# Performance work log

Hardware: AMD Instinct MI355X
Metric: run time of the kernel (lower is better)

## Reference

```python
import jax, jax.numpy as jnp
import numpy as np

NODELEN = 394
N_NODES = 50000
N_EDGES = 200000
IN_DIM = 2 * NODELEN  # 788
H2 = 192
EMB = 128


def setup_inputs() -> dict:
    key = jax.random.key(0)
    ks = jax.random.split(key, 12)
    inp = {
        'features': jax.random.normal(ks[0], (N_NODES, NODELEN), dtype=jnp.float32),
        'src': jax.random.randint(ks[1], (N_EDGES,), 0, N_NODES),
        'dst': jax.random.randint(ks[2], (N_EDGES,), 0, N_NODES),
        # AutoEncoder params (Linear weights stored as [in, out])
        'W_enc1': jax.random.normal(ks[3], (IN_DIM, H2), dtype=jnp.float32) / np.sqrt(IN_DIM),
        'b_enc1': jnp.zeros((H2,), dtype=jnp.float32),
        'W_enc3': jax.random.normal(ks[4], (H2, EMB), dtype=jnp.float32) / np.sqrt(H2),
        'b_enc3': jnp.zeros((EMB,), dtype=jnp.float32),
        'W_dec1': jax.random.normal(ks[5], (EMB, H2), dtype=jnp.float32) / np.sqrt(EMB),
        'b_dec1': jnp.zeros((H2,), dtype=jnp.float32),
        'W_dec3': jax.random.normal(ks[6], (H2, IN_DIM), dtype=jnp.float32) / np.sqrt(H2),
        'b_dec3': jnp.zeros((IN_DIM,), dtype=jnp.float32),
    }
    return inp


def _segment_mean(msgs, dst, inv_deg, n):
    # msgs: [E, F] gathered neighbor features; mean over incoming edges per node
    return jax.ops.segment_sum(msgs, dst, num_segments=n) * inv_deg


def reference(features, src, dst, W_enc1, b_enc1, W_enc3, b_enc3,
              W_dec1, b_dec1, W_dec3, b_dec3):
    n = features.shape[0]
    ones = jnp.ones(src.shape[0], dtype=features.dtype)
    deg = jax.ops.segment_sum(ones, dst, num_segments=n)
    # nodes with no neighbors fall back to the zero dummy vector (as in source)
    inv_deg = (1.0 / jnp.maximum(deg, 1.0))[:, None]

    # depth-1 aggregation: mean of raw neighbor features, then feat[0] := 0
    h1 = _segment_mean(features[src], dst, inv_deg, n)
    h1 = h1.at[:, 0].set(0.0)
    # depth-2 aggregation: mean of depth-1 aggregates of neighbors, feat[0] := 0
    h2 = _segment_mean(h1[src], dst, inv_deg, n)
    h2 = h2.at[:, 0].set(0.0)

    # concatenated embedding with positions 0 and NODELEN zeroed
    emb = jnp.concatenate([features, h2], axis=1)  # [N, 788]
    emb = emb.at[:, 0].set(0.0).at[:, NODELEN].set(0.0)

    # AutoEncoder forward (dropout is identity at inference)
    x = jax.nn.relu(emb @ W_enc1 + b_enc1)
    encoded = x @ W_enc3 + b_enc3
    y = jax.nn.relu(encoded @ W_dec1 + b_dec1)
    decoded = y @ W_dec3 + b_dec3
    return encoded, decoded, emb
```

## Files before the change

kernel.cpp:

```cpp
#include <hip/hip_runtime.h>
#include <hip/hip_bf16.h>

#define NODELEN 394
#define IN_DIM 788
#define H2DIM 192
#define EMBDIM 128
#define NCHUNK 197

typedef __attribute__((ext_vector_type(4))) float f32x4;
typedef __attribute__((ext_vector_type(8))) short bfrag;

#define LBAR() do { asm volatile("s_waitcnt lgkmcnt(0)" ::: "memory"); \
                    __builtin_amdgcn_s_barrier(); } while (0)

static __device__ __forceinline__ unsigned short f2bf(float f) {
    union { float f; unsigned u; } v; v.f = f;
    unsigned r = v.u + 0x7FFFu + ((v.u >> 16) & 1u);
    return (unsigned short)(r >> 16);
}
static __device__ __forceinline__ float bf2f(unsigned short h) {
    union { unsigned u; float f; } v; v.u = ((unsigned)h) << 16;
    return v.f;
}
static __device__ __forceinline__ unsigned short f2bf_fast(float f) {
    __hip_bfloat16 h = __float2bfloat16(f);
    union { __hip_bfloat16 h; unsigned short u; } c; c.h = h; return c.u;
}


__global__ void count_deg(const int* __restrict__ dst, int* __restrict__ deg, int e) {
    int i = blockIdx.x * blockDim.x + threadIdx.x;
    if (i < e) atomicAdd(&deg[dst[i]], 1);
}

__global__ void block_sum(const int* __restrict__ deg, int* __restrict__ bsum, int n) {
    __shared__ int s[256];
    int t = threadIdx.x;
    int i = blockIdx.x * 256 + t;
    s[t] = (i < n) ? deg[i] : 0;
    __syncthreads();
    for (int d = 128; d > 0; d >>= 1) {
        if (t < d) s[t] += s[t + d];
        __syncthreads();
    }
    if (t == 0) bsum[blockIdx.x] = s[0];
}

__global__ void scan_bsums(int* bsum, int nb) {
    __shared__ int s[256];
    int t = threadIdx.x;
    int x0 = (t < nb) ? bsum[t] : 0;
    s[t] = x0;
    __syncthreads();
    for (int d = 1; d < 256; d <<= 1) {
        int u = (t >= d) ? s[t - d] : 0;
        __syncthreads();
        s[t] += u;
        __syncthreads();
    }
    if (t < nb) bsum[t] = s[t] - x0;
}

__global__ void block_scan(const int* __restrict__ deg, const int* __restrict__ boff,
                           int* __restrict__ rowstart, int* __restrict__ cursor,
                           float* __restrict__ inv, int n) {
    __shared__ int s[256];
    int t = threadIdx.x;
    int i = blockIdx.x * 256 + t;
    int x0 = (i < n) ? deg[i] : 0;
    s[t] = x0;
    __syncthreads();
    for (int d = 1; d < 256; d <<= 1) {
        int u = (t >= d) ? s[t - d] : 0;
        __syncthreads();
        s[t] += u;
        __syncthreads();
    }
    if (i < n) {
        int r = boff[blockIdx.x] + s[t] - x0;
        rowstart[i] = r;
        cursor[i] = r;
        inv[i] = 1.0f / fmaxf((float)x0, 1.0f);
    }
}

__global__ void fill_edges(const int* __restrict__ src, const int* __restrict__ dst,
                           int* __restrict__ cursor, int* __restrict__ elist, int e) {
    int i = blockIdx.x * blockDim.x + threadIdx.x;
    if (i < e) {
        int p = atomicAdd(&cursor[dst[i]], 1);
        elist[p] = src[i];
    }
}


__global__ __launch_bounds__(256) void gather1(
        const float* __restrict__ feat, const int* __restrict__ rowstart,
        const int* __restrict__ deg, const float* __restrict__ inv,
        const int* __restrict__ elist, unsigned short* __restrict__ h1) {
    const int node = blockIdx.x;
    const int c = threadIdx.x;
    if (c >= NCHUNK) return;
    const int beg = rowstart[node];
    const int dc = deg[node];
    const float s = inv[node];
    const size_t off = (size_t)c * 2;

    float ax = 0.f, ay = 0.f, bx = 0.f, by = 0.f;
    float cx = 0.f, cy = 0.f, dx = 0.f, dy = 0.f;
    int j = 0;
    for (; j + 3 < dc; j += 4) {
        int n0 = elist[beg + j], n1 = elist[beg + j + 1];
        int n2 = elist[beg + j + 2], n3 = elist[beg + j + 3];
        float2 v0 = *(const float2*)(feat + (size_t)n0 * NODELEN + off);
        float2 v1 = *(const float2*)(feat + (size_t)n1 * NODELEN + off);
        float2 v2 = *(const float2*)(feat + (size_t)n2 * NODELEN + off);
        float2 v3 = *(const float2*)(feat + (size_t)n3 * NODELEN + off);
        ax += v0.x; ay += v0.y; bx += v1.x; by += v1.y;
        cx += v2.x; cy += v2.y; dx += v3.x; dy += v3.y;
    }
    for (; j < dc; ++j) {
        int n0 = elist[beg + j];
        float2 v0 = *(const float2*)(feat + (size_t)n0 * NODELEN + off);
        ax += v0.x; ay += v0.y;
    }
    float fx = (ax + bx + cx + dx) * s;
    float fy = (ay + by + cy + dy) * s;
    if (c == 0) fx = 0.f;
    unsigned out = ((unsigned)f2bf(fy) << 16) | (unsigned)f2bf(fx);
    *(unsigned*)(h1 + (size_t)node * NODELEN + off) = out;
}

__global__ __launch_bounds__(256) void gather2_emb(
        const float* __restrict__ feat, const unsigned* __restrict__ h1,
        const int* __restrict__ rowstart, const int* __restrict__ deg,
        const float* __restrict__ inv, const int* __restrict__ elist,
        float* __restrict__ emb, unsigned* __restrict__ emb16u) {
    const int node = blockIdx.x;
    const int c = threadIdx.x;
    if (c >= NCHUNK) return;
    const int beg = rowstart[node];
    const int dc = deg[node];
    const float s = inv[node];

    float ax = 0.f, ay = 0.f, bx = 0.f, by = 0.f;
    float cx = 0.f, cy = 0.f, dx = 0.f, dy = 0.f;
    int j = 0;
    for (; j + 3 < dc; j += 4) {
        int n0 = elist[beg + j], n1 = elist[beg + j + 1];
        int n2 = elist[beg + j + 2], n3 = elist[beg + j + 3];
        unsigned u0 = h1[(size_t)n0 * NCHUNK + c];
        unsigned u1 = h1[(size_t)n1 * NCHUNK + c];
        unsigned u2 = h1[(size_t)n2 * NCHUNK + c];
        unsigned u3 = h1[(size_t)n3 * NCHUNK + c];
        ax += bf2f((unsigned short)u0); ay += bf2f((unsigned short)(u0 >> 16));
        bx += bf2f((unsigned short)u1); by += bf2f((unsigned short)(u1 >> 16));
        cx += bf2f((unsigned short)u2); cy += bf2f((unsigned short)(u2 >> 16));
        dx += bf2f((unsigned short)u3); dy += bf2f((unsigned short)(u3 >> 16));
    }
    for (; j < dc; ++j) {
        int n0 = elist[beg + j];
        unsigned u0 = h1[(size_t)n0 * NCHUNK + c];
        ax += bf2f((unsigned short)u0); ay += bf2f((unsigned short)(u0 >> 16));
    }
    float hx = (ax + bx + cx + dx) * s;
    float hy = (ay + by + cy + dy) * s;

    const float* fr = feat + (size_t)node * NODELEN;
    float* er = emb + (size_t)node * IN_DIM;
    float2 fv = *(const float2*)(fr + c * 2);
    if (c == 0) { fv.x = 0.f; hx = 0.f; }
    *(float2*)(er + c * 2) = fv;
    float2 hv; hv.x = hx; hv.y = hy;
    *(float2*)(er + NODELEN + c * 2) = hv;

    if (emb16u) {
        unsigned* e16 = emb16u + (size_t)node * 400;
        e16[c]          = ((unsigned)f2bf(fv.y) << 16) | (unsigned)f2bf(fv.x);
        e16[NCHUNK + c] = ((unsigned)f2bf(hy)  << 16) | (unsigned)f2bf(hx);
        if (c < 6) e16[394 + c] = 0u;
    }
}

__device__ __forceinline__ void tr_one(const float* W, unsigned short* Wt,
                                       int K, int N, int Kp, int idx) {
    int nrow = idx / Kp, k = idx - nrow * Kp;
    Wt[idx] = (k < K) ? f2bf(W[(size_t)k * N + nrow]) : (unsigned short)0;
}

#define T1E (192 * 800)
#define T2E (128 * 192)
#define T3E (192 * 128)
#define T4E (788 * 192)

__global__ void transpose_all(const float* __restrict__ W1, unsigned short* __restrict__ Wt1,
                              const float* __restrict__ W2, unsigned short* __restrict__ Wt2,
                              const float* __restrict__ W3, unsigned short* __restrict__ Wt3,
                              const float* __restrict__ W4, unsigned short* __restrict__ Wt4) {
    int idx = blockIdx.x * 256 + threadIdx.x;
    if (idx < T1E) { tr_one(W1, Wt1, IN_DIM, H2DIM, 800, idx); return; }
    idx -= T1E;
    if (idx < T2E) { tr_one(W2, Wt2, H2DIM, EMBDIM, 192, idx); return; }
    idx -= T2E;
    if (idx < T3E) { tr_one(W3, Wt3, EMBDIM, H2DIM, 128, idx); return; }
    idx -= T3E;
    if (idx < T4E) { tr_one(W4, Wt4, H2DIM, IN_DIM, 192, idx); return; }
}

static __device__ __forceinline__ int bs_addr(int r, int s) {
    return r * 32 + ((s ^ ((r >> 1) & 3)) << 3);
}
static __device__ __forceinline__ int xy_base(int r, int s) {
    int ph = (s & 24) | ((s ^ r) & 7);
    return r * 192 + (ph << 3);
}
static __device__ __forceinline__ int xy_addr_s(int r, int col) { return xy_base(r, col >> 3) + (col & 7); }

static __device__ __forceinline__ bfrag load_af_bf(const unsigned short* A800, int gm, int M, int col) {
    const bfrag zf = {0, 0, 0, 0, 0, 0, 0, 0};
    return (gm < M) ? *(const bfrag*)(A800 + (size_t)gm * 800 + col) : zf;
}
static __device__ __forceinline__ bfrag load_af_f32(const float* A, int gm, int M, int col) {
    float t[8];
    #pragma unroll
    for (int q = 0; q < 8; ++q) t[q] = 0.f;
    if (gm < M) {
        const float* rp = A + (size_t)gm * IN_DIM;
        if (col + 8 <= IN_DIM) {
            float4 v0 = *(const float4*)(rp + col), v1 = *(const float4*)(rp + col + 4);
            t[0] = v0.x; t[1] = v0.y; t[2] = v0.z; t[3] = v0.w;
            t[4] = v1.x; t[5] = v1.y; t[6] = v1.z; t[7] = v1.w;
        } else {
            #pragma unroll
            for (int q = 0; q < 8; ++q) if (col + q < IN_DIM) t[q] = rp[col + q];
        }
    }
    union { unsigned short u[8]; bfrag v; } pk;
    #pragma unroll
    for (int q = 0; q < 8; ++q) pk.u[q] = f2bf_fast(t[q]);
    return pk.v;
}

template <int ABF>
__global__ __launch_bounds__(256, 2) void mlp12(
    const void* __restrict__ Aemb,
    const unsigned short* __restrict__ Wt1,
    const unsigned short* __restrict__ Wt2,
    const float* __restrict__ b1, const float* __restrict__ b2,
    float* __restrict__ encoded, unsigned short* __restrict__ enc16, int M)
{
    __shared__ unsigned short XY[128 * 192];
    __shared__ unsigned short Bs[2][192 * 32];

    const int tid = threadIdx.x;
    const int wid = tid >> 6, l = tid & 63;
    const int wm = wid >> 1, wn = wid & 1;
    const int lr = l & 15, lk = l >> 4;
    const int m0 = blockIdx.x * 128;

    const int r0 = tid >> 2, s0 = tid & 3;
    const int r1 = r0 + 64, r2 = r0 + 128;
    const int bw0 = bs_addr(r0, s0);
    const int bw1 = bs_addr(r1, s0);
    const int bw2 = bs_addr(r2, s0);
    int brd6[6], brd4[4];
    #pragma unroll
    for (int j = 0; j < 6; ++j) brd6[j] = bs_addr(wn * 96 + j * 16 + lr, lk);
    #pragma unroll
    for (int j = 0; j < 4; ++j) brd4[j] = bs_addr(wn * 64 + j * 16 + lr, lk);

    int gmA[4];
    #pragma unroll
    for (int i = 0; i < 4; ++i) gmA[i] = m0 + wm * 64 + i * 16 + lr;

    {
        f32x4 acc[4][6];
        #pragma unroll
        for (int i = 0; i < 4; ++i)
            #pragma unroll
            for (int j = 0; j < 6; ++j) acc[i][j] = (f32x4){0.f, 0.f, 0.f, 0.f};

        bfrag afC[4], afN[4], bN[3];
        #pragma unroll
        for (int i = 0; i < 4; ++i)
            afC[i] = ABF ? load_af_bf((const unsigned short*)Aemb, gmA[i], M, lk * 8)
                         : load_af_f32((const float*)Aemb, gmA[i], M, lk * 8);
        *(bfrag*)&Bs[0][bw0] = *(const bfrag*)(Wt1 + (size_t)r0 * 800 + s0 * 8);
        *(bfrag*)&Bs[0][bw1] = *(const bfrag*)(Wt1 + (size_t)r1 * 800 + s0 * 8);
        *(bfrag*)&Bs[0][bw2] = *(const bfrag*)(Wt1 + (size_t)r2 * 800 + s0 * 8);
        LBAR();

        #pragma unroll 5
        for (int kt = 0; kt < 25; ++kt) {
            if (kt < 24) {
                int k0 = (kt + 1) * 32;
                #pragma unroll
                for (int i = 0; i < 4; ++i)
                    afN[i] = ABF ? load_af_bf((const unsigned short*)Aemb, gmA[i], M, k0 + lk * 8)
                                 : load_af_f32((const float*)Aemb, gmA[i], M, k0 + lk * 8);
                bN[0] = *(const bfrag*)(Wt1 + (size_t)r0 * 800 + k0 + s0 * 8);
                bN[1] = *(const bfrag*)(Wt1 + (size_t)r1 * 800 + k0 + s0 * 8);
                bN[2] = *(const bfrag*)(Wt1 + (size_t)r2 * 800 + k0 + s0 * 8);
            }
            const unsigned short* B = Bs[kt & 1];
            bfrag bf[6];
            #pragma unroll
            for (int j = 0; j < 6; ++j) bf[j] = *(const bfrag*)&B[brd6[j]];
            #pragma unroll
            for (int i = 0; i < 4; ++i)
                #pragma unroll
                for (int j = 0; j < 6; ++j)
                    acc[i][j] = __builtin_amdgcn_mfma_f32_16x16x32_bf16(afC[i], bf[j], acc[i][j], 0, 0, 0);
            if (kt < 24) {
                unsigned short* Bn = Bs[(kt + 1) & 1];
                *(bfrag*)&Bn[bw0] = bN[0];
                *(bfrag*)&Bn[bw1] = bN[1];
                *(bfrag*)&Bn[bw2] = bN[2];
                LBAR();
                #pragma unroll
                for (int i = 0; i < 4; ++i) afC[i] = afN[i];
            }
        }
        float bv[6];
        #pragma unroll
        for (int j = 0; j < 6; ++j) bv[j] = b1[wn * 96 + j * 16 + lr];
        #pragma unroll
        for (int i = 0; i < 4; ++i)
            #pragma unroll
            for (int j = 0; j < 6; ++j)
                #pragma unroll
                for (int r = 0; r < 4; ++r) {
                    int m = wm * 64 + i * 16 + lk * 4 + r;
                    int n1 = wn * 96 + j * 16 + lr;
                    XY[xy_addr_s(m, n1)] = f2bf_fast(fmaxf(acc[i][j][r] + bv[j], 0.f));
                }
    }
    __syncthreads();

    {
        f32x4 acc[4][4];
        #pragma unroll
        for (int i = 0; i < 4; ++i)
            #pragma unroll
            for (int j = 0; j < 4; ++j) acc[i][j] = (f32x4){0.f, 0.f, 0.f, 0.f};

        bfrag bN[2];
        *(bfrag*)&Bs[0][bw0] = *(const bfrag*)(Wt2 + (size_t)r0 * 192 + s0 * 8);
        *(bfrag*)&Bs[0][bw1] = *(const bfrag*)(Wt2 + (size_t)r1 * 192 + s0 * 8);
        LBAR();

        #pragma unroll
        for (int kt = 0; kt < 6; ++kt) {
            if (kt < 5) {
                int k0 = (kt + 1) * 32;
                bN[0] = *(const bfrag*)(Wt2 + (size_t)r0 * 192 + k0 + s0 * 8);
                bN[1] = *(const bfrag*)(Wt2 + (size_t)r1 * 192 + k0 + s0 * 8);
            }
            const unsigned short* B = Bs[kt & 1];
            bfrag af[4], bf[4];
            #pragma unroll
            for (int i = 0; i < 4; ++i)
                af[i] = *(const bfrag*)&XY[xy_base(wm * 64 + i * 16 + lr, kt * 4 + lk)];
            #pragma unroll
            for (int j = 0; j < 4; ++j) bf[j] = *(const bfrag*)&B[brd4[j]];
            #pragma unroll
            for (int i = 0; i < 4; ++i)
                #pragma unroll
                for (int j = 0; j < 4; ++j)
                    acc[i][j] = __builtin_amdgcn_mfma_f32_16x16x32_bf16(af[i], bf[j], acc[i][j], 0, 0, 0);
            if (kt < 5) {
                unsigned short* Bn = Bs[(kt + 1) & 1];
                *(bfrag*)&Bn[bw0] = bN[0];
                *(bfrag*)&Bn[bw1] = bN[1];
                LBAR();
            }
        }

        float bv[4];
        #pragma unroll
        for (int j = 0; j < 4; ++j) bv[j] = b2[wn * 64 + j * 16 + lr];
        #pragma unroll
        for (int i = 0; i < 4; ++i)
            #pragma unroll
            for (int j = 0; j < 4; ++j)
                #pragma unroll
                for (int r = 0; r < 4; ++r) {
                    int m = wm * 64 + i * 16 + lk * 4 + r;
                    int nn = wn * 64 + j * 16 + lr;
                    float v = acc[i][j][r] + bv[j];
                    int gm = m0 + m;
                    if (gm < M) {
                        encoded[(size_t)gm * EMBDIM + nn] = v;
                        enc16[(size_t)gm * EMBDIM + nn] = f2bf_fast(v);
                    }
                }
    }
}

__global__ __launch_bounds__(256, 2) void mlp34(
    const unsigned short* __restrict__ enc16,
    const unsigned short* __restrict__ Wt3,
    const unsigned short* __restrict__ Wt4,
    const float* __restrict__ b3, const float* __restrict__ b4,
    float* __restrict__ decoded, int M)
{
    __shared__ unsigned short XY[128 * 192];
    __shared__ unsigned short Bs[2][192 * 32];

    const int tid = threadIdx.x;
    const int wid = tid >> 6, l = tid & 63;
    const int wm = wid >> 1, wn = wid & 1;
    const int lr = l & 15, lk = l >> 4;
    const int m0 = blockIdx.x * 128;
    const bfrag zf = {0, 0, 0, 0, 0, 0, 0, 0};

    const int r0 = tid >> 2, s0 = tid & 3;
    const int r1 = r0 + 64, r2 = r0 + 128;
    const int bw0 = bs_addr(r0, s0);
    const int bw1 = bs_addr(r1, s0);
    const int bw2 = bs_addr(r2, s0);
    int brd6[6], brd4[4];
    #pragma unroll
    for (int j = 0; j < 6; ++j) brd6[j] = bs_addr(wn * 96 + j * 16 + lr, lk);
    #pragma unroll
    for (int j = 0; j < 4; ++j) brd4[j] = bs_addr(wn * 64 + j * 16 + lr, lk);

    int gmA[4];
    #pragma unroll
    for (int i = 0; i < 4; ++i) gmA[i] = m0 + wm * 64 + i * 16 + lr;

    {
        f32x4 acc[4][6];
        #pragma unroll
        for (int i = 0; i < 4; ++i)
            #pragma unroll
            for (int j = 0; j < 6; ++j) acc[i][j] = (f32x4){0.f, 0.f, 0.f, 0.f};

        bfrag afC[4], afN[4], bN[3];
        #pragma unroll
        for (int i = 0; i < 4; ++i)
            afC[i] = (gmA[i] < M) ? *(const bfrag*)(enc16 + (size_t)gmA[i] * EMBDIM + lk * 8) : zf;
        *(bfrag*)&Bs[0][bw0] = *(const bfrag*)(Wt3 + (size_t)r0 * 128 + s0 * 8);
        *(bfrag*)&Bs[0][bw1] = *(const bfrag*)(Wt3 + (size_t)r1 * 128 + s0 * 8);
        *(bfrag*)&Bs[0][bw2] = *(const bfrag*)(Wt3 + (size_t)r2 * 128 + s0 * 8);
        LBAR();

        #pragma unroll
        for (int kt = 0; kt < 4; ++kt) {
            if (kt < 3) {
                int k0 = (kt + 1) * 32;
                #pragma unroll
                for (int i = 0; i < 4; ++i)
                    afN[i] = (gmA[i] < M)
                        ? *(const bfrag*)(enc16 + (size_t)gmA[i] * EMBDIM + k0 + lk * 8) : zf;
                bN[0] = *(const bfrag*)(Wt3 + (size_t)r0 * 128 + k0 + s0 * 8);
                bN[1] = *(const bfrag*)(Wt3 + (size_t)r1 * 128 + k0 + s0 * 8);
                bN[2] = *(const bfrag*)(Wt3 + (size_t)r2 * 128 + k0 + s0 * 8);
            }
            const unsigned short* B = Bs[kt & 1];
            bfrag bf[6];
            #pragma unroll
            for (int j = 0; j < 6; ++j) bf[j] = *(const bfrag*)&B[brd6[j]];
            #pragma unroll
            for (int i = 0; i < 4; ++i)
                #pragma unroll
                for (int j = 0; j < 6; ++j)
                    acc[i][j] = __builtin_amdgcn_mfma_f32_16x16x32_bf16(afC[i], bf[j], acc[i][j], 0, 0, 0);
            if (kt < 3) {
                unsigned short* Bn = Bs[(kt + 1) & 1];
                *(bfrag*)&Bn[bw0] = bN[0];
                *(bfrag*)&Bn[bw1] = bN[1];
                *(bfrag*)&Bn[bw2] = bN[2];
                LBAR();
                #pragma unroll
                for (int i = 0; i < 4; ++i) afC[i] = afN[i];
            }
        }

        float bv[6];
        #pragma unroll
        for (int j = 0; j < 6; ++j) bv[j] = b3[wn * 96 + j * 16 + lr];
        #pragma unroll
        for (int i = 0; i < 4; ++i)
            #pragma unroll
            for (int j = 0; j < 6; ++j)
                #pragma unroll
                for (int r = 0; r < 4; ++r) {
                    int m = wm * 64 + i * 16 + lk * 4 + r;
                    int nc = wn * 96 + j * 16 + lr;
                    XY[xy_addr_s(m, nc)] = f2bf_fast(fmaxf(acc[i][j][r] + bv[j], 0.f));
                }
    }
    __syncthreads();

    {
        bfrag af4[6][4];
        #pragma unroll
        for (int q = 0; q < 6; ++q)
            #pragma unroll
            for (int i = 0; i < 4; ++i)
                af4[q][i] = *(const bfrag*)&XY[xy_base(wm * 64 + i * 16 + lr, q * 4 + lk)];

        bfrag bN[2];
        *(bfrag*)&Bs[0][bw0] = *(const bfrag*)(Wt4 + (size_t)r0 * 192 + s0 * 8);
        *(bfrag*)&Bs[0][bw1] = *(const bfrag*)(Wt4 + (size_t)r1 * 192 + s0 * 8);
        LBAR();

        for (int nc = 0; nc < 7; ++nc) {
            f32x4 acc[4][4];
            #pragma unroll
            for (int i = 0; i < 4; ++i)
                #pragma unroll
                for (int j = 0; j < 4; ++j) acc[i][j] = (f32x4){0.f, 0.f, 0.f, 0.f};

            #pragma unroll
            for (int kt = 0; kt < 6; ++kt) {
                const bool last = (nc == 6) && (kt == 5);
                if (!last) {
                    int nn = (kt < 5) ? nc : nc + 1;
                    int nk = (kt < 5) ? (kt + 1) * 32 : 0;
                    int g0 = nn * 128 + r0, g1 = nn * 128 + r1;
                    bN[0] = (g0 < IN_DIM) ? *(const bfrag*)(Wt4 + (size_t)g0 * 192 + nk + s0 * 8) : zf;
                    bN[1] = (g1 < IN_DIM) ? *(const bfrag*)(Wt4 + (size_t)g1 * 192 + nk + s0 * 8) : zf;
                }
                const unsigned short* B = Bs[kt & 1];
                bfrag bf[4];
                #pragma unroll
                for (int j = 0; j < 4; ++j) bf[j] = *(const bfrag*)&B[brd4[j]];
                #pragma unroll
                for (int i = 0; i < 4; ++i)
                    #pragma unroll
                    for (int j = 0; j < 4; ++j)
                        acc[i][j] = __builtin_amdgcn_mfma_f32_16x16x32_bf16(af4[kt][i], bf[j], acc[i][j], 0, 0, 0);
                if (!last) {
                    unsigned short* Bn = Bs[(kt + 1) & 1];
                    *(bfrag*)&Bn[bw0] = bN[0];
                    *(bfrag*)&Bn[bw1] = bN[1];
                    LBAR();
                }
            }

            float bv[4];
            #pragma unroll
            for (int j = 0; j < 4; ++j) {
                int nn = nc * 128 + wn * 64 + j * 16 + lr;
                bv[j] = (nn < IN_DIM) ? b4[nn] : 0.f;
            }
            #pragma unroll
            for (int i = 0; i < 4; ++i)
                #pragma unroll
                for (int j = 0; j < 4; ++j)
                    #pragma unroll
                    for (int r = 0; r < 4; ++r) {
                        int gm = m0 + wm * 64 + i * 16 + lk * 4 + r;
                        int nn = nc * 128 + wn * 64 + j * 16 + lr;
                        if (gm < M && nn < IN_DIM)
                            decoded[(size_t)gm * IN_DIM + nn] = acc[i][j][r] + bv[j];
                    }
        }
    }
}


extern "C" void kernel_launch(void* const* d_in, const int* in_sizes, int n_in,
                              void* d_out, int out_size, void* d_ws, size_t ws_size,
                              hipStream_t stream) {
    const float* features = (const float*)d_in[0];
    const int*   src      = (const int*)d_in[1];
    const int*   dst      = (const int*)d_in[2];
    const float* W_enc1   = (const float*)d_in[3];
    const float* b_enc1   = (const float*)d_in[4];
    const float* W_enc3   = (const float*)d_in[5];
    const float* b_enc3   = (const float*)d_in[6];
    const float* W_dec1   = (const float*)d_in[7];
    const float* b_dec1   = (const float*)d_in[8];
    const float* W_dec3   = (const float*)d_in[9];
    const float* b_dec3   = (const float*)d_in[10];

    const int n = in_sizes[0] / NODELEN;
    const int e = in_sizes[1];

    float* encoded = (float*)d_out;
    float* decoded = encoded + (size_t)n * EMBDIM;
    float* emb     = decoded + (size_t)n * IN_DIM;

    char* ws = (char*)d_ws;
    unsigned short* h1    = (unsigned short*)(ws + 0);
    unsigned short* enc16 = (unsigned short*)(ws + 0);
    unsigned short* Wt1 = (unsigned short*)(ws + 40000000);
    unsigned short* Wt2 = (unsigned short*)(ws + 40400000);
    unsigned short* Wt3 = (unsigned short*)(ws + 40500000);
    unsigned short* Wt4 = (unsigned short*)(ws + 40600000);
    float* inv          = (float*)(ws + 41000000);
    int*   deg          = (int*)  (ws + 41200000);
    int*   rowstart     = (int*)  (ws + 41400000);
    int*   cursor       = (int*)  (ws + 41600000);
    int*   elist        = (int*)  (ws + 41800000);
    int*   bsum         = (int*)  (ws + 42600000);
    unsigned short* emb16 = (unsigned short*)(ws + 44000000);
    const size_t NEED = 44000000ull + (size_t)n * 800 * 2;
    const int useBF = (ws_size >= NEED) ? 1 : 0;

    const int nb = (n + 255) / 256;
    const int eb = (e + 255) / 256;

    transpose_all<<<(T1E + T2E + T3E + T4E + 255) / 256, 256, 0, stream>>>(
        W_enc1, Wt1, W_enc3, Wt2, W_dec1, Wt3, W_dec3, Wt4);

    hipMemsetAsync(deg, 0, (size_t)n * sizeof(int), stream);
    count_deg<<<eb, 256, 0, stream>>>(dst, deg, e);
    block_sum<<<nb, 256, 0, stream>>>(deg, bsum, n);
    scan_bsums<<<1, 256, 0, stream>>>(bsum, nb);
    block_scan<<<nb, 256, 0, stream>>>(deg, bsum, rowstart, cursor, inv, n);
    fill_edges<<<eb, 256, 0, stream>>>(src, dst, cursor, elist, e);

    gather1<<<n, 256, 0, stream>>>(features, rowstart, deg, inv, elist, h1);
    gather2_emb<<<n, 256, 0, stream>>>(features, (const unsigned*)h1, rowstart, deg,
                                       inv, elist, emb,
                                       useBF ? (unsigned*)emb16 : nullptr);

    const int MB = (n + 127) / 128;
    if (useBF) {
        mlp12<1><<<MB, 256, 0, stream>>>(emb16, Wt1, Wt2, b_enc1, b_enc3, encoded, enc16, n);
    } else {
        mlp12<0><<<MB, 256, 0, stream>>>(emb, Wt1, Wt2, b_enc1, b_enc3, encoded, enc16, n);
    }
    mlp34<<<MB, 256, 0, stream>>>(enc16, Wt3, Wt4, b_dec1, b_dec3, decoded, n);
}
```

Measured before the change: 341.1 us.

## Flatten gather kernels into grid-stride loops and deepen GEMM prefetch to two stages

The two gather kernels stop using one 256-thread block per node, which left 59 of 256 threads idle. They now run a grid-stride loop over node*chunk indices on a fixed grid of 2048 blocks, so every lane does work and far fewer blocks are launched. All four MLP GEMM loops now prefetch global tiles two k-steps ahead into registers instead of one, to hide more global-load latency behind the MFMAs. The deeper prefetch costs extra registers, which may lower occupancy, and the flattened gather gives up per-node uniformity of deg and rowstart within a wavefront.

```diff
diff --git a/kernel.cpp b/kernel.cpp
--- a/kernel.cpp
+++ b/kernel.cpp
@@ -97,88 +97,90 @@
 __global__ __launch_bounds__(256) void gather1(
         const float* __restrict__ feat, const int* __restrict__ rowstart,
         const int* __restrict__ deg, const float* __restrict__ inv,
-        const int* __restrict__ elist, unsigned short* __restrict__ h1) {
-    const int node = blockIdx.x;
-    const int c = threadIdx.x;
-    if (c >= NCHUNK) return;
-    const int beg = rowstart[node];
-    const int dc = deg[node];
-    const float s = inv[node];
-    const size_t off = (size_t)c * 2;
-
-    float ax = 0.f, ay = 0.f, bx = 0.f, by = 0.f;
-    float cx = 0.f, cy = 0.f, dx = 0.f, dy = 0.f;
-    int j = 0;
-    for (; j + 3 < dc; j += 4) {
-        int n0 = elist[beg + j], n1 = elist[beg + j + 1];
-        int n2 = elist[beg + j + 2], n3 = elist[beg + j + 3];
-        float2 v0 = *(const float2*)(feat + (size_t)n0 * NODELEN + off);
-        float2 v1 = *(const float2*)(feat + (size_t)n1 * NODELEN + off);
-        float2 v2 = *(const float2*)(feat + (size_t)n2 * NODELEN + off);
-        float2 v3 = *(const float2*)(feat + (size_t)n3 * NODELEN + off);
-        ax += v0.x; ay += v0.y; bx += v1.x; by += v1.y;
-        cx += v2.x; cy += v2.y; dx += v3.x; dy += v3.y;
-    }
-    for (; j < dc; ++j) {
-        int n0 = elist[beg + j];
-        float2 v0 = *(const float2*)(feat + (size_t)n0 * NODELEN + off);
-        ax += v0.x; ay += v0.y;
-    }
-    float fx = (ax + bx + cx + dx) * s;
-    float fy = (ay + by + cy + dy) * s;
-    if (c == 0) fx = 0.f;
-    unsigned out = ((unsigned)f2bf(fy) << 16) | (unsigned)f2bf(fx);
-    *(unsigned*)(h1 + (size_t)node * NODELEN + off) = out;
+        const int* __restrict__ elist, unsigned short* __restrict__ h1, int total) {
+    for (int idx = blockIdx.x * 256 + threadIdx.x; idx < total; idx += gridDim.x * 256) {
+        const int node = idx / NCHUNK;
+        const int c = idx - node * NCHUNK;
+        const int beg = rowstart[node];
+        const int dc = deg[node];
+        const float s = inv[node];
+        const size_t off = (size_t)c * 2;
+
+        float ax = 0.f, ay = 0.f, bx = 0.f, by = 0.f;
+        float cx = 0.f, cy = 0.f, dx = 0.f, dy = 0.f;
+        int j = 0;
+        for (; j + 3 < dc; j += 4) {
+            int n0 = elist[beg + j], n1 = elist[beg + j + 1];
+            int n2 = elist[beg + j + 2], n3 = elist[beg + j + 3];
+            float2 v0 = *(const float2*)(feat + (size_t)n0 * NODELEN + off);
+            float2 v1 = *(const float2*)(feat + (size_t)n1 * NODELEN + off);
+            float2 v2 = *(const float2*)(feat + (size_t)n2 * NODELEN + off);
+            float2 v3 = *(const float2*)(feat + (size_t)n3 * NODELEN + off);
+            ax += v0.x; ay += v0.y; bx += v1.x; by += v1.y;
+            cx += v2.x; cy += v2.y; dx += v3.x; dy += v3.y;
+        }
+        for (; j < dc; ++j) {
+            int n0 = elist[beg + j];
+            float2 v0 = *(const float2*)(feat + (size_t)n0 * NODELEN + off);
+            ax += v0.x; ay += v0.y;
+        }
+        float fx = (ax + bx + cx + dx) * s;
+        float fy = (ay + by + cy + dy) * s;
+        if (c == 0) fx = 0.f;
+        unsigned out = ((unsigned)f2bf(fy) << 16) | (unsigned)f2bf(fx);
+        *(unsigned*)(h1 + (size_t)node * NODELEN + off) = out;
+    }
 }
 
 __global__ __launch_bounds__(256) void gather2_emb(
         const float* __restrict__ feat, const unsigned* __restrict__ h1,
         const int* __restrict__ rowstart, const int* __restrict__ deg,
         const float* __restrict__ inv, const int* __restrict__ elist,
-        float* __restrict__ emb, unsigned* __restrict__ emb16u) {
-    const int node = blockIdx.x;
-    const int c = threadIdx.x;
-    if (c >= NCHUNK) return;
-    const int beg = rowstart[node];
-    const int dc = deg[node];
-    const float s = inv[node];
-
-    float ax = 0.f, ay = 0.f, bx = 0.f, by = 0.f;
-    float cx = 0.f, cy = 0.f, dx = 0.f, dy = 0.f;
-    int j = 0;
-    for (; j + 3 < dc; j += 4) {
-        int n0 = elist[beg + j], n1 = elist[beg + j + 1];
-        int n2 = elist[beg + j + 2], n3 = elist[beg + j + 3];
-        unsigned u0 = h1[(size_t)n0 * NCHUNK + c];
-        unsigned u1 = h1[(size_t)n1 * NCHUNK + c];
-        unsigned u2 = h1[(size_t)n2 * NCHUNK + c];
-        unsigned u3 = h1[(size_t)n3 * NCHUNK + c];
-        ax += bf2f((unsigned short)u0); ay += bf2f((unsigned short)(u0 >> 16));
-        bx += bf2f((unsigned short)u1); by += bf2f((unsigned short)(u1 >> 16));
-        cx += bf2f((unsigned short)u2); cy += bf2f((unsigned short)(u2 >> 16));
-        dx += bf2f((unsigned short)u3); dy += bf2f((unsigned short)(u3 >> 16));
-    }
-    for (; j < dc; ++j) {
-        int n0 = elist[beg + j];
-        unsigned u0 = h1[(size_t)n0 * NCHUNK + c];
-        ax += bf2f((unsigned short)u0); ay += bf2f((unsigned short)(u0 >> 16));
-    }
-    float hx = (ax + bx + cx + dx) * s;
-    float hy = (ay + by + cy + dy) * s;
-
-    const float* fr = feat + (size_t)node * NODELEN;
-    float* er = emb + (size_t)node * IN_DIM;
-    float2 fv = *(const float2*)(fr + c * 2);
-    if (c == 0) { fv.x = 0.f; hx = 0.f; }
-    *(float2*)(er + c * 2) = fv;
-    float2 hv; hv.x = hx; hv.y = hy;
-    *(float2*)(er + NODELEN + c * 2) = hv;
-
-    if (emb16u) {
-        unsigned* e16 = emb16u + (size_t)node * 400;
-        e16[c]          = ((unsigned)f2bf(fv.y) << 16) | (unsigned)f2bf(fv.x);
-        e16[NCHUNK + c] = ((unsigned)f2bf(hy)  << 16) | (unsigned)f2bf(hx);
-        if (c < 6) e16[394 + c] = 0u;
+        float* __restrict__ emb, unsigned* __restrict__ emb16u, int total) {
+    for (int idx = blockIdx.x * 256 + threadIdx.x; idx < total; idx += gridDim.x * 256) {
+        const int node = idx / NCHUNK;
+        const int c = idx - node * NCHUNK;
+        const int beg = rowstart[node];
+        const int dc = deg[node];
+        const float s = inv[node];
+
+        float ax = 0.f, ay = 0.f, bx = 0.f, by = 0.f;
+        float cx = 0.f, cy = 0.f, dx = 0.f, dy = 0.f;
+        int j = 0;
+        for (; j + 3 < dc; j += 4) {
+            int n0 = elist[beg + j], n1 = elist[beg + j + 1];
+            int n2 = elist[beg + j + 2], n3 = elist[beg + j + 3];
+            unsigned u0 = h1[(size_t)n0 * NCHUNK + c];
+            unsigned u1 = h1[(size_t)n1 * NCHUNK + c];
+            unsigned u2 = h1[(size_t)n2 * NCHUNK + c];
+            unsigned u3 = h1[(size_t)n3 * NCHUNK + c];
+            ax += bf2f((unsigned short)u0); ay += bf2f((unsigned short)(u0 >> 16));
+            bx += bf2f((unsigned short)u1); by += bf2f((unsigned short)(u1 >> 16));
+            cx += bf2f((unsigned short)u2); cy += bf2f((unsigned short)(u2 >> 16));
+            dx += bf2f((unsigned short)u3); dy += bf2f((unsigned short)(u3 >> 16));
+        }
+        for (; j < dc; ++j) {
+            int n0 = elist[beg + j];
+            unsigned u0 = h1[(size_t)n0 * NCHUNK + c];
+            ax += bf2f((unsigned short)u0); ay += bf2f((unsigned short)(u0 >> 16));
+        }
+        float hx = (ax + bx + cx + dx) * s;
+        float hy = (ay + by + cy + dy) * s;
+
+        const float* fr = feat + (size_t)node * NODELEN;
+        float* er = emb + (size_t)node * IN_DIM;
+        float2 fv = *(const float2*)(fr + c * 2);
+        if (c == 0) { fv.x = 0.f; hx = 0.f; }
+        *(float2*)(er + c * 2) = fv;
+        float2 hv; hv.x = hx; hv.y = hy;
+        *(float2*)(er + NODELEN + c * 2) = hv;
+
+        if (emb16u) {
+            unsigned* e16 = emb16u + (size_t)node * 400;
+            e16[c]          = ((unsigned)f2bf(fv.y) << 16) | (unsigned)f2bf(fv.x);
+            e16[NCHUNK + c] = ((unsigned)f2bf(hy)  << 16) | (unsigned)f2bf(hx);
+            if (c < 6) e16[394 + c] = 0u;
+        }
     }
 }
 
@@ -280,27 +282,33 @@
             #pragma unroll
             for (int j = 0; j < 6; ++j) acc[i][j] = (f32x4){0.f, 0.f, 0.f, 0.f};
 
-        bfrag afC[4], afN[4], bN[3];
-        #pragma unroll
-        for (int i = 0; i < 4; ++i)
+        bfrag afC[4], afN[4], afN2[4], bR1[3], bR2[3];
+        #pragma unroll
+        for (int i = 0; i < 4; ++i) {
             afC[i] = ABF ? load_af_bf((const unsigned short*)Aemb, gmA[i], M, lk * 8)
                          : load_af_f32((const float*)Aemb, gmA[i], M, lk * 8);
+            afN[i] = ABF ? load_af_bf((const unsigned short*)Aemb, gmA[i], M, 32 + lk * 8)
+                         : load_af_f32((const float*)Aemb, gmA[i], M, 32 + lk * 8);
+        }
         *(bfrag*)&Bs[0][bw0] = *(const bfrag*)(Wt1 + (size_t)r0 * 800 + s0 * 8);
         *(bfrag*)&Bs[0][bw1] = *(const bfrag*)(Wt1 + (size_t)r1 * 800 + s0 * 8);
         *(bfrag*)&Bs[0][bw2] = *(const bfrag*)(Wt1 + (size_t)r2 * 800 + s0 * 8);
+        bR1[0] = *(const bfrag*)(Wt1 + (size_t)r0 * 800 + 32 + s0 * 8);
+        bR1[1] = *(const bfrag*)(Wt1 + (size_t)r1 * 800 + 32 + s0 * 8);
+        bR1[2] = *(const bfrag*)(Wt1 + (size_t)r2 * 800 + 32 + s0 * 8);
         LBAR();
 
         #pragma unroll 5
         for (int kt = 0; kt < 25; ++kt) {
-            if (kt < 24) {
-                int k0 = (kt + 1) * 32;
+            if (kt < 23) {
+                int k2 = (kt + 2) * 32;
                 #pragma unroll
                 for (int i = 0; i < 4; ++i)
-                    afN[i] = ABF ? load_af_bf((const unsigned short*)Aemb, gmA[i], M, k0 + lk * 8)
-                                 : load_af_f32((const float*)Aemb, gmA[i], M, k0 + lk * 8);
-                bN[0] = *(const bfrag*)(Wt1 + (size_t)r0 * 800 + k0 + s0 * 8);
-                bN[1] = *(const bfrag*)(Wt1 + (size_t)r1 * 800 + k0 + s0 * 8);
-                bN[2] = *(const bfrag*)(Wt1 + (size_t)r2 * 800 + k0 + s0 * 8);
+                    afN2[i] = ABF ? load_af_bf((const unsigned short*)Aemb, gmA[i], M, k2 + lk * 8)
+                                  : load_af_f32((const float*)Aemb, gmA[i], M, k2 + lk * 8);
+                bR2[0] = *(const bfrag*)(Wt1 + (size_t)r0 * 800 + k2 + s0 * 8);
+                bR2[1] = *(const bfrag*)(Wt1 + (size_t)r1 * 800 + k2 + s0 * 8);
+                bR2[2] = *(const bfrag*)(Wt1 + (size_t)r2 * 800 + k2 + s0 * 8);
             }
             const unsigned short* B = Bs[kt & 1];
             bfrag bf[6];
@@ -313,12 +321,13 @@
                     acc[i][j] = __builtin_amdgcn_mfma_f32_16x16x32_bf16(afC[i], bf[j], acc[i][j], 0, 0, 0);
             if (kt < 24) {
                 unsigned short* Bn = Bs[(kt + 1) & 1];
-                *(bfrag*)&Bn[bw0] = bN[0];
-                *(bfrag*)&Bn[bw1] = bN[1];
-                *(bfrag*)&Bn[bw2] = bN[2];
+                *(bfrag*)&Bn[bw0] = bR1[0];
+                *(bfrag*)&Bn[bw1] = bR1[1];
+                *(bfrag*)&Bn[bw2] = bR1[2];
                 LBAR();
                 #pragma unroll
-                for (int i = 0; i < 4; ++i) afC[i] = afN[i];
+                for (int i = 0; i < 4; ++i) { afC[i] = afN[i]; afN[i] = afN2[i]; }
+                bR1[0] = bR2[0]; bR1[1] = bR2[1]; bR1[2] = bR2[2];
             }
         }
         float bv[6];
@@ -344,17 +353,19 @@
             #pragma unroll
             for (int j = 0; j < 4; ++j) acc[i][j] = (f32x4){0.f, 0.f, 0.f, 0.f};
 
-        bfrag bN[2];
+        bfrag bR1[2], bR2[2];
         *(bfrag*)&Bs[0][bw0] = *(const bfrag*)(Wt2 + (size_t)r0 * 192 + s0 * 8);
         *(bfrag*)&Bs[0][bw1] = *(const bfrag*)(Wt2 + (size_t)r1 * 192 + s0 * 8);
+        bR1[0] = *(const bfrag*)(Wt2 + (size_t)r0 * 192 + 32 + s0 * 8);
+        bR1[1] = *(const bfrag*)(Wt2 + (size_t)r1 * 192 + 32 + s0 * 8);
         LBAR();
 
         #pragma unroll
         for (int kt = 0; kt < 6; ++kt) {
-            if (kt < 5) {
-                int k0 = (kt + 1) * 32;
-                bN[0] = *(const bfrag*)(Wt2 + (size_t)r0 * 192 + k0 + s0 * 8);
-                bN[1] = *(const bfrag*)(Wt2 + (size_t)r1 * 192 + k0 + s0 * 8);
+            if (kt < 4) {
+                int k2 = (kt + 2) * 32;
+                bR2[0] = *(const bfrag*)(Wt2 + (size_t)r0 * 192 + k2 + s0 * 8);
+                bR2[1] = *(const bfrag*)(Wt2 + (size_t)r1 * 192 + k2 + s0 * 8);
             }
             const unsigned short* B = Bs[kt & 1];
             bfrag af[4], bf[4];
@@ -370,9 +381,10 @@
                     acc[i][j] = __builtin_amdgcn_mfma_f32_16x16x32_bf16(af[i], bf[j], acc[i][j], 0, 0, 0);
             if (kt < 5) {
                 unsigned short* Bn = Bs[(kt + 1) & 1];
-                *(bfrag*)&Bn[bw0] = bN[0];
-                *(bfrag*)&Bn[bw1] = bN[1];
+                *(bfrag*)&Bn[bw0] = bR1[0];
+                *(bfrag*)&Bn[bw1] = bR1[1];
                 LBAR();
+                bR1[0] = bR2[0]; bR1[1] = bR2[1];
             }
         }
 
@@ -436,26 +448,31 @@
             #pragma unroll
             for (int j = 0; j < 6; ++j) acc[i][j] = (f32x4){0.f, 0.f, 0.f, 0.f};
 
-        bfrag afC[4], afN[4], bN[3];
-        #pragma unroll
-        for (int i = 0; i < 4; ++i)
+        bfrag afC[4], afN[4], afN2[4], bR1[3], bR2[3];
+        #pragma unroll
+        for (int i = 0; i < 4; ++i) {
             afC[i] = (gmA[i] < M) ? *(const bfrag*)(enc16 + (size_t)gmA[i] * EMBDIM + lk * 8) : zf;
+            afN[i] = (gmA[i] < M) ? *(const bfrag*)(enc16 + (size_t)gmA[i] * EMBDIM + 32 + lk * 8) : zf;
+        }
         *(bfrag*)&Bs[0][bw0] = *(const bfrag*)(Wt3 + (size_t)r0 * 128 + s0 * 8);
         *(bfrag*)&Bs[0][bw1] = *(const bfrag*)(Wt3 + (size_t)r1 * 128 + s0 * 8);
         *(bfrag*)&Bs[0][bw2] = *(const bfrag*)(Wt3 + (size_t)r2 * 128 + s0 * 8);
+        bR1[0] = *(const bfrag*)(Wt3 + (size_t)r0 * 128 + 32 + s0 * 8);
+        bR1[1] = *(const bfrag*)(Wt3 + (size_t)r1 * 128 + 32 + s0 * 8);
+        bR1[2] = *(const bfrag*)(Wt3 + (size_t)r2 * 128 + 32 + s0 * 8);
         LBAR();
 
         #pragma unroll
         for (int kt = 0; kt < 4; ++kt) {
-            if (kt < 3) {
-                int k0 = (kt + 1) * 32;
+            if (kt < 2) {
+                int k2 = (kt + 2) * 32;
                 #pragma unroll
                 for (int i = 0; i < 4; ++i)
-                    afN[i] = (gmA[i] < M)
-                        ? *(const bfrag*)(enc16 + (size_t)gmA[i] * EMBDIM + k0 + lk * 8) : zf;
-                bN[0] = *(const bfrag*)(Wt3 + (size_t)r0 * 128 + k0 + s0 * 8);
-                bN[1] = *(const bfrag*)(Wt3 + (size_t)r1 * 128 + k0 + s0 * 8);
-                bN[2] = *(const bfrag*)(Wt3 + (size_t)r2 * 128 + k0 + s0 * 8);
+                    afN2[i] = (gmA[i] < M)
+                        ? *(const bfrag*)(enc16 + (size_t)gmA[i] * EMBDIM + k2 + lk * 8) : zf;
+                bR2[0] = *(const bfrag*)(Wt3 + (size_t)r0 * 128 + k2 + s0 * 8);
+                bR2[1] = *(const bfrag*)(Wt3 + (size_t)r1 * 128 + k2 + s0 * 8);
+                bR2[2] = *(const bfrag*)(Wt3 + (size_t)r2 * 128 + k2 + s0 * 8);
             }
             const unsigned short* B = Bs[kt & 1];
             bfrag bf[6];
@@ -468,12 +485,13 @@
                     acc[i][j] = __builtin_amdgcn_mfma_f32_16x16x32_bf16(afC[i], bf[j], acc[i][j], 0, 0, 0);
             if (kt < 3) {
                 unsigned short* Bn = Bs[(kt + 1) & 1];
-                *(bfrag*)&Bn[bw0] = bN[0];
-                *(bfrag*)&Bn[bw1] = bN[1];
-                *(bfrag*)&Bn[bw2] = bN[2];
+                *(bfrag*)&Bn[bw0] = bR1[0];
+                *(bfrag*)&Bn[bw1] = bR1[1];
+                *(bfrag*)&Bn[bw2] = bR1[2];
                 LBAR();
                 #pragma unroll
-                for (int i = 0; i < 4; ++i) afC[i] = afN[i];
+                for (int i = 0; i < 4; ++i) { afC[i] = afN[i]; afN[i] = afN2[i]; }
+                bR1[0] = bR2[0]; bR1[1] = bR2[1]; bR1[2] = bR2[2];
             }
         }
 
@@ -501,9 +519,11 @@
             for (int i = 0; i < 4; ++i)
                 af4[q][i] = *(const bfrag*)&XY[xy_base(wm * 64 + i * 16 + lr, q * 4 + lk)];
 
-        bfrag bN[2];
+        bfrag bR1[2], bR2[2];
         *(bfrag*)&Bs[0][bw0] = *(const bfrag*)(Wt4 + (size_t)r0 * 192 + s0 * 8);
         *(bfrag*)&Bs[0][bw1] = *(const bfrag*)(Wt4 + (size_t)r1 * 192 + s0 * 8);
+        bR1[0] = *(const bfrag*)(Wt4 + (size_t)r0 * 192 + 32 + s0 * 8);
+        bR1[1] = *(const bfrag*)(Wt4 + (size_t)r1 * 192 + 32 + s0 * 8);
         LBAR();
 
         for (int nc = 0; nc < 7; ++nc) {
@@ -515,15 +535,15 @@
 
             #pragma unroll
             for (int kt = 0; kt < 6; ++kt) {
-                const bool last = (nc == 6) && (kt == 5);
-                if (!last) {
-                    int nn = (kt < 5) ? nc : nc + 1;
-                    int nk = (kt < 5) ? (kt + 1) * 32 : 0;
-                    int g0 = nn * 128 + r0, g1 = nn * 128 + r1;
-                    bN[0] = (g0 < IN_DIM) ? *(const bfrag*)(Wt4 + (size_t)g0 * 192 + nk + s0 * 8) : zf;
-                    bN[1] = (g1 < IN_DIM) ? *(const bfrag*)(Wt4 + (size_t)g1 * 192 + nk + s0 * 8) : zf;
+                const int t = nc * 6 + kt;
+                if (t < 40) {
+                    int nn2 = (kt < 4) ? nc : nc + 1;
+                    int nk2 = ((kt + 2) % 6) * 32;
+                    int g0 = nn2 * 128 + r0, g1 = nn2 * 128 + r1;
+                    bR2[0] = (g0 < IN_DIM) ? *(const bfrag*)(Wt4 + (size_t)g0 * 192 + nk2 + s0 * 8) : zf;
+                    bR2[1] = (g1 < IN_DIM) ? *(const bfrag*)(Wt4 + (size_t)g1 * 192 + nk2 + s0 * 8) : zf;
                 }
-                const unsigned short* B = Bs[kt & 1];
+                const unsigned short* B = Bs[t & 1];
                 bfrag bf[4];
                 #pragma unroll
                 for (int j = 0; j < 4; ++j) bf[j] = *(const bfrag*)&B[brd4[j]];
@@ -532,11 +552,12 @@
                     #pragma unroll
                     for (int j = 0; j < 4; ++j)
                         acc[i][j] = __builtin_amdgcn_mfma_f32_16x16x32_bf16(af4[kt][i], bf[j], acc[i][j], 0, 0, 0);
-                if (!last) {
-                    unsigned short* Bn = Bs[(kt + 1) & 1];
-                    *(bfrag*)&Bn[bw0] = bN[0];
-                    *(bfrag*)&Bn[bw1] = bN[1];
+                if (t < 41) {
+                    unsigned short* Bn = Bs[(t + 1) & 1];
+                    *(bfrag*)&Bn[bw0] = bR1[0];
+                    *(bfrag*)&Bn[bw1] = bR1[1];
                     LBAR();
+                    bR1[0] = bR2[0]; bR1[1] = bR2[1];
                 }
             }
 
@@ -603,6 +624,7 @@
 
     const int nb = (n + 255) / 256;
     const int eb = (e + 255) / 256;
+    const int total = n * NCHUNK;
 
     transpose_all<<<(T1E + T2E + T3E + T4E + 255) / 256, 256, 0, stream>>>(
         W_enc1, Wt1, W_enc3, Wt2, W_dec1, Wt3, W_dec3, Wt4);
@@ -614,10 +636,10 @@
     block_scan<<<nb, 256, 0, stream>>>(deg, bsum, rowstart, cursor, inv, n);
     fill_edges<<<eb, 256, 0, stream>>>(src, dst, cursor, elist, e);
 
-    gather1<<<n, 256, 0, stream>>>(features, rowstart, deg, inv, elist, h1);
-    gather2_emb<<<n, 256, 0, stream>>>(features, (const unsigned*)h1, rowstart, deg,
-                                       inv, elist, emb,
-                                       useBF ? (unsigned*)emb16 : nullptr);
+    gather1<<<2048, 256, 0, stream>>>(features, rowstart, deg, inv, elist, h1, total);
+    gather2_emb<<<2048, 256, 0, stream>>>(features, (const unsigned*)h1, rowstart, deg,
+                                          inv, elist, emb,
+                                          useBF ? (unsigned*)emb16 : nullptr, total);
 
     const int MB = (n + 127) / 128;
     if (useBF) {
```

Measured after the change: 370.4 us. 1.09x slower.
